# Kernel tuning notes

Hardware: AMD Instinct MI355X
Metric: run time of the kernel (lower is better)

Reference implementation:

```python
import jax, jax.numpy as jnp
import numpy as np

N = 8192        # number of nodes (adjacency is N x N)
F_IN = 256      # in_features
F_OUT = 256     # out_features


def setup_inputs() -> dict:
    key = jax.random.key(0)
    k_x, k_adj, k_kernel, k_bias, k_beta = jax.random.split(key, 5)
    x = jax.random.normal(k_x, (N, F_IN), dtype=jnp.float32)
    adj = jax.random.uniform(k_adj, (N, N), dtype=jnp.float32)  # dense non-negative adjacency buffer
    # xavier-uniform-like scale for the kernel
    limit = float(np.sqrt(6.0 / (F_IN + F_OUT)))
    kernel = jax.random.uniform(k_kernel, (F_IN, F_OUT), dtype=jnp.float32, minval=-limit, maxval=limit)
    bias = 0.01 * jax.random.normal(k_bias, (F_OUT,), dtype=jnp.float32)
    beta = 0.01 * jax.random.normal(k_beta, (N,), dtype=jnp.float32)
    return {"x": x, "adj": adj, "kernel": kernel, "bias": bias, "beta": beta}


def reference(x, adj, kernel, bias, beta):
    # Original: diag(1/(rowsum(adj)+beta)) @ (adj + diag(beta)) @ x @ kernel + bias
    # Fused form: row-scale and diagonal-add applied without materializing NxN diag matrices.
    scale = jnp.reciprocal(jnp.sum(adj, axis=1) + beta)          # [N]
    agg = adj @ x + beta[:, None] * x                             # (adj + diag(beta)) @ x  -> [N, F_IN]
    return (scale[:, None] * agg) @ kernel + bias                 # [N, F_OUT]
```

## Files before the change

kernel.cpp:

```cpp
#include <hip/hip_runtime.h>
#include <hip/hip_bf16.h>


typedef __attribute__((ext_vector_type(8))) short  short8;
typedef __attribute__((ext_vector_type(4))) short  bf16x4;
typedef __attribute__((ext_vector_type(4))) float  floatx4;

#define N_NODES 8192
#define F_DIM   256
#define BK      64
#define NSTEPS  (N_NODES / BK)

#define ASYNC16(g, l)                                                          \
  __builtin_amdgcn_global_load_lds(                                           \
      (const __attribute__((address_space(1))) void*)(g),                     \
      (__attribute__((address_space(3))) void*)(l), 16, 0, 0)

__device__ __forceinline__ unsigned short f2bf(float f) {
  unsigned u = __float_as_uint(f);
  return (unsigned short)((u + 0x7FFFu + ((u >> 16) & 1u)) >> 16);
}

__device__ __forceinline__ short8 pack_bf16x8(floatx4 a, floatx4 b) {
  short8 r;
  r[0] = (short)f2bf(a.x);
  r[1] = (short)f2bf(a.y);
  r[2] = (short)f2bf(a.z);
  r[3] = (short)f2bf(a.w);
  r[4] = (short)f2bf(b.x);
  r[5] = (short)f2bf(b.y);
  r[6] = (short)f2bf(b.z);
  r[7] = (short)f2bf(b.w);
  return r;
}

__global__ __launch_bounds__(256) void tile_bf16_kernel(
    const float* __restrict__ src, unsigned short* __restrict__ dst, int K) {
  const int Nn = F_DIM;
  int cid = blockIdx.x * 256 + threadIdx.x;
  int per_kblk = Nn * 4;
  int kblk = cid / per_kblk;
  int rem  = cid - kblk * per_kblk;
  int n16 = rem >> 6;
  int kg  = (rem >> 4) & 3;
  int nl  = rem & 15;
  int n = n16 * 16 + nl;
  int k = kblk * 32 + kg * 8;
  const float* s = src + (size_t)k * Nn + n;
  floatx4 v0, v1;
  v0.x = s[0];
  v0.y = s[(size_t)Nn];
  v0.z = s[(size_t)2 * Nn];
  v0.w = s[(size_t)3 * Nn];
  v1.x = s[(size_t)4 * Nn];
  v1.y = s[(size_t)5 * Nn];
  v1.z = s[(size_t)6 * Nn];
  v1.w = s[(size_t)7 * Nn];
  *(short8*)(dst + (size_t)cid * 8) = pack_bf16x8(v0, v1);
}

#define MFMA16(a, b, c) __builtin_amdgcn_mfma_f32_16x16x32_bf16(a, b, c, 0, 0, 0)
#define AB(c) (smem + (c) * 4096)

#define LOADB(dst, sv)                                                         \
  _Pragma("unroll") for (int kb_ = 0; kb_ < 2; ++kb_)                          \
  _Pragma("unroll") for (int nf_ = 0; nf_ < 2; ++nf_)                          \
      dst[kb_][nf_] = *(const short8*)(bgl + (size_t)(sv) * 16384 +            \
                                       kb_ * 8192 + nf_ * 512);

#define COPYB()                                                                \
  _Pragma("unroll") for (int kb_ = 0; kb_ < 2; ++kb_)                          \
  _Pragma("unroll") for (int nf_ = 0; nf_ < 2; ++nf_) bc[kb_][nf_] = bn[kb_][nf_];

#define WRITE_A(cw)                                                            \
  {                                                                            \
    rsum += (areg_w.x + areg_w.y) + (areg_w.z + areg_w.w);                     \
    bf16x4 pk_;                                                                \
    pk_[0] = (short)f2bf(areg_w.x);                                            \
    pk_[1] = (short)f2bf(areg_w.y);                                            \
    pk_[2] = (short)f2bf(areg_w.z);                                            \
    pk_[3] = (short)f2bf(areg_w.w);                                            \
    *(bf16x4*)(AB(cw) + awoff) = pk_;                                          \
  }

#define COMPUTE(c)                                                             \
  {                                                                            \
    const char* Ab_ = AB(c);                                                   \
    short8 a00 = *(const short8*)(Ab_ + aoff00);                \
    short8 a01 = *(const short8*)(Ab_ + aoff01);                \
    short8 a10 = *(const short8*)(Ab_ + aoff10);                \
    short8 a11 = *(const short8*)(Ab_ + aoff11);                \
    acc[0][0] = MFMA16(a00, bc[0][0], acc[0][0]);                              \
    acc[0][1] = MFMA16(a00, bc[0][1], acc[0][1]);                              \
    acc[1][0] = MFMA16(a10, bc[0][0], acc[1][0]);                              \
    acc[1][1] = MFMA16(a10, bc[0][1], acc[1][1]);                              \
    acc[0][0] = MFMA16(a01, bc[1][0], acc[0][0]);                              \
    acc[0][1] = MFMA16(a01, bc[1][1], acc[0][1]);                              \
    acc[1][0] = MFMA16(a11, bc[1][0], acc[1][0]);                              \
    acc[1][1] = MFMA16(a11, bc[1][1], acc[1][1]);                              \
  }

#define FULL_ITER(sv, c, cw)                                                   \
  LOADB(bn, (sv) + 1);                                                         \
  areg_l = *(const floatx4*)(agl + (size_t)((sv) + 2) * BK);                   \
  asm volatile("s_waitcnt lgkmcnt(0)\n\ts_barrier" ::: "memory");              \
  WRITE_A(cw);                                                                 \
  COMPUTE(c);                                                                  \
  COPYB();                                                                     \
  areg_w = areg_l;

__global__ __launch_bounds__(512, 2) void fused_kernel(
    const float* __restrict__ adj, const unsigned short* __restrict__ xbt,
    const float* __restrict__ x, const float* __restrict__ beta,
    const float* __restrict__ bias, const unsigned short* __restrict__ wbt,
    float* __restrict__ out) {
  __shared__ __attribute__((aligned(16))) char smem[49408];
  float* sscale = (float*)(smem + 49152);
  float* sbeta  = (float*)(smem + 49280);

  const int tid = threadIdx.x;
  const int w   = tid >> 6;
  const int l   = tid & 63;
  const int kq  = l >> 4;
  const int ml  = l & 15;
  const int m0  = blockIdx.x * 32;

  const int arow = tid >> 4;
  const int ag4  = tid & 15;
  const float* agl = adj + (size_t)(m0 + arow) * N_NODES + ag4 * 4;
  const int awoff = arow * 128 + (((ag4 >> 1) ^ (arow & 7)) << 4) + (ag4 & 1) * 8;

  const int aoff00 = (0 * 16 + ml) * 128 + (((0 * 4 + kq) ^ (ml & 7)) << 4);
  const int aoff01 = (0 * 16 + ml) * 128 + (((1 * 4 + kq) ^ (ml & 7)) << 4);
  const int aoff10 = (1 * 16 + ml) * 128 + (((0 * 4 + kq) ^ (ml & 7)) << 4);
  const int aoff11 = (1 * 16 + ml) * 128 + (((1 * 4 + kq) ^ (ml & 7)) << 4);

  const unsigned short* bgl = xbt + w * 1024 + kq * 128 + ml * 8;

  floatx4 acc[2][2];
  const floatx4 zf4 = {0.f, 0.f, 0.f, 0.f};
  acc[0][0] = zf4; acc[0][1] = zf4; acc[1][0] = zf4; acc[1][1] = zf4;
  float rsum = 0.f;
  floatx4 areg_w, areg_l;
  short8 bc[2][2], bn[2][2];

  {
    floatx4 a0v = *(const floatx4*)(agl);
    LOADB(bc, 0);
    areg_w = *(const floatx4*)(agl + BK);
    rsum += (a0v.x + a0v.y) + (a0v.z + a0v.w);
    bf16x4 pk;
    pk[0] = (short)f2bf(a0v.x);
    pk[1] = (short)f2bf(a0v.y);
    pk[2] = (short)f2bf(a0v.z);
    pk[3] = (short)f2bf(a0v.w);
    *(bf16x4*)(AB(0) + awoff) = pk;
  }

  for (int t = 0; t < 42; ++t) {
    const int s0 = 3 * t;
    FULL_ITER(s0,     0, 1);
    FULL_ITER(s0 + 1, 1, 2);
    FULL_ITER(s0 + 2, 2, 0);
  }
  LOADB(bn, 127);
  asm volatile("s_waitcnt lgkmcnt(0)\n\ts_barrier" ::: "memory");
  WRITE_A(1);
  COMPUTE(0);
  COPYB();
  asm volatile("s_waitcnt lgkmcnt(0)\n\ts_barrier" ::: "memory");
  COMPUTE(1);

  __syncthreads();

  {
    const float* xs = x + (size_t)m0 * F_DIM + tid * 4;
    char* xd = smem + 16384 + (w << 10);
#pragma unroll
    for (int q = 0; q < 4; ++q) ASYNC16(xs + q * 2048, xd + q * 8192);
  }
  {
    float rs = rsum;
    rs += __shfl_xor(rs, 1);
    rs += __shfl_xor(rs, 2);
    rs += __shfl_xor(rs, 4);
    rs += __shfl_xor(rs, 8);
    if ((l & 15) == 0) {
      int row = w * 4 + (l >> 4);
      float b = beta[m0 + row];
      sbeta[row]  = b;
      sscale[row] = 1.0f / (rs + b);
    }
  }
  __syncthreads();

  const float* xl = (const float*)(smem + 16384);
  unsigned short* G = (unsigned short*)smem;
#pragma unroll
  for (int nf = 0; nf < 2; ++nf) {
    int col = w * 32 + nf * 16 + ml;
    int chunk = col >> 3;
#pragma unroll
    for (int mf = 0; mf < 2; ++mf)
#pragma unroll
      for (int r = 0; r < 4; ++r) {
        int row = mf * 16 + kq * 4 + r;
        float g = sscale[row] * (acc[mf][nf][r] + sbeta[row] * xl[row * F_DIM + col]);
        int slot = (chunk & 24) | ((chunk ^ row) & 7);
        G[row * 256 + slot * 8 + (col & 7)] = f2bf(g);
      }
  }
  __syncthreads();

  floatx4 acc2[2][2];
  acc2[0][0] = zf4; acc2[0][1] = zf4; acc2[1][0] = zf4; acc2[1][1] = zf4;
#pragma unroll
  for (int s2 = 0; s2 < 8; ++s2) {
    int c = s2 * 4 + kq;
    int sl = (c & 24) | ((c ^ ml) & 7);
    short8 ag0 = *(const short8*)(G + (ml)      * 256 + sl * 8);
    short8 ag1 = *(const short8*)(G + (16 + ml) * 256 + sl * 8);
    const unsigned short* wb = wbt + s2 * 8192 + (w * 2) * 512 + kq * 128 + ml * 8;
    short8 wv0 = *(const short8*)(wb);
    short8 wv1 = *(const short8*)(wb + 512);
    acc2[0][0] = MFMA16(ag0, wv0, acc2[0][0]);
    acc2[1][0] = MFMA16(ag1, wv0, acc2[1][0]);
    acc2[0][1] = MFMA16(ag0, wv1, acc2[0][1]);
    acc2[1][1] = MFMA16(ag1, wv1, acc2[1][1]);
  }
#pragma unroll
  for (int nf = 0; nf < 2; ++nf) {
    int col = w * 32 + nf * 16 + ml;
    float bv = bias[col];
#pragma unroll
    for (int mf = 0; mf < 2; ++mf)
#pragma unroll
      for (int r = 0; r < 4; ++r) {
        int row = m0 + mf * 16 + kq * 4 + r;
        out[(size_t)row * F_DIM + col] = acc2[mf][nf][r] + bv;
      }
  }
}

extern "C" void kernel_launch(void* const* d_in, const int* in_sizes, int n_in,
                              void* d_out, int out_size, void* d_ws, size_t ws_size,
                              hipStream_t stream) {
  const float* x    = (const float*)d_in[0];
  const float* adj  = (const float*)d_in[1];
  const float* kern = (const float*)d_in[2];
  const float* bias = (const float*)d_in[3];
  const float* beta = (const float*)d_in[4];
  float* out = (float*)d_out;

  char* ws = (char*)d_ws;
  unsigned short* xbt = (unsigned short*)ws;
  unsigned short* wbt = xbt + (size_t)N_NODES * F_DIM;

  tile_bf16_kernel<<<(N_NODES * F_DIM / 8) / 256, 256, 0, stream>>>(x, xbt, N_NODES);
  tile_bf16_kernel<<<(F_DIM * F_DIM / 8) / 256, 256, 0, stream>>>(kern, wbt, F_DIM);
  fused_kernel<<<256, 512, 0, stream>>>(adj, xbt, x, beta, bias, wbt, out);
}
```

Before: 428.5 us.

## Quadruple K-tile depth of adjacency GEMM pipeline and stream B fragments per sub-step

Raises the K tile from 64 to 256, so each barrier-separated stage stages a 32x256 bf16 slice of the adjacency in LDS with a new swizzle, and the main loop drops from 128 steps to 32. Each stage now runs eight MFMA sub-steps, loading B (the pre-transposed bf16 x) from global just-in-time, one sub-step ahead, instead of prefetching a whole stage of B into registers. The aim is fewer barriers and longer MFMA runs per barrier. In exchange the kernel needs about 48KB of LDS for the A buffers, launch bounds drop to one block per CU, and the per-sub-step global B loads may expose latency.

```diff
diff --git a/kernel.cpp b/kernel.cpp
--- a/kernel.cpp
+++ b/kernel.cpp
@@ -3,12 +3,11 @@
 
 
 typedef __attribute__((ext_vector_type(8))) short  short8;
-typedef __attribute__((ext_vector_type(4))) short  bf16x4;
 typedef __attribute__((ext_vector_type(4))) float  floatx4;
 
 #define N_NODES 8192
 #define F_DIM   256
-#define BK      64
+#define BK      256
 #define NSTEPS  (N_NODES / BK)
 
 #define ASYNC16(g, l)                                                          \
@@ -60,56 +59,65 @@
 }
 
 #define MFMA16(a, b, c) __builtin_amdgcn_mfma_f32_16x16x32_bf16(a, b, c, 0, 0, 0)
-#define AB(c) (smem + (c) * 4096)
-
-#define LOADB(dst, sv)                                                         \
-  _Pragma("unroll") for (int kb_ = 0; kb_ < 2; ++kb_)                          \
-  _Pragma("unroll") for (int nf_ = 0; nf_ < 2; ++nf_)                          \
-      dst[kb_][nf_] = *(const short8*)(bgl + (size_t)(sv) * 16384 +            \
-                                       kb_ * 8192 + nf_ * 512);
-
-#define COPYB()                                                                \
-  _Pragma("unroll") for (int kb_ = 0; kb_ < 2; ++kb_)                          \
-  _Pragma("unroll") for (int nf_ = 0; nf_ < 2; ++nf_) bc[kb_][nf_] = bn[kb_][nf_];
+#define AB(c)  (smem + (c) * 16384)
+#define LDB(p) (*(const short8*)(p))
+#define BS(sv) (bgl + (size_t)(sv) * 65536)
+
+#define AOFF(mf, kb)                                                           \
+  (((mf) * 16 + ml) * 512 +                                                    \
+   (((((kb) * 4 + kq) & 24) | ((((kb) * 4 + kq) ^ ml) & 7)) << 4))
 
 #define WRITE_A(cw)                                                            \
   {                                                                            \
-    rsum += (areg_w.x + areg_w.y) + (areg_w.z + areg_w.w);                     \
-    bf16x4 pk_;                                                                \
-    pk_[0] = (short)f2bf(areg_w.x);                                            \
-    pk_[1] = (short)f2bf(areg_w.y);                                            \
-    pk_[2] = (short)f2bf(areg_w.z);                                            \
-    pk_[3] = (short)f2bf(areg_w.w);                                            \
-    *(bf16x4*)(AB(cw) + awoff) = pk_;                                          \
-  }
-
-#define COMPUTE(c)                                                             \
+    rsum += ((aw0.x + aw0.y) + (aw0.z + aw0.w)) +                              \
+            ((aw1.x + aw1.y) + (aw1.z + aw1.w)) +                              \
+            ((aw2.x + aw2.y) + (aw2.z + aw2.w)) +                              \
+            ((aw3.x + aw3.y) + (aw3.z + aw3.w));                               \
+    *(short8*)(AB(cw) + awoff0) = pack_bf16x8(aw0, aw1);                       \
+    *(short8*)(AB(cw) + awoff1) = pack_bf16x8(aw2, aw3);                       \
+  }
+
+#define KB(kb)                                                                 \
+  a0_ = *(const short8*)(Ab_ + AOFF(0, kb));                                   \
+  a1_ = *(const short8*)(Ab_ + AOFF(1, kb));                                   \
+  n0_ = LDB(Bsv_ + ((kb) + 1) * 8192);                                         \
+  n1_ = LDB(Bsv_ + ((kb) + 1) * 8192 + 512);                                   \
+  acc[0][0] = MFMA16(a0_, b0_, acc[0][0]);                                     \
+  acc[0][1] = MFMA16(a0_, b1_, acc[0][1]);                                     \
+  acc[1][0] = MFMA16(a1_, b0_, acc[1][0]);                                     \
+  acc[1][1] = MFMA16(a1_, b1_, acc[1][1]);                                     \
+  b0_ = n0_; b1_ = n1_;
+
+#define KBLAST(kb)                                                             \
+  a0_ = *(const short8*)(Ab_ + AOFF(0, kb));                                   \
+  a1_ = *(const short8*)(Ab_ + AOFF(1, kb));                                   \
+  acc[0][0] = MFMA16(a0_, b0_, acc[0][0]);                                     \
+  acc[0][1] = MFMA16(a0_, b1_, acc[0][1]);                                     \
+  acc[1][0] = MFMA16(a1_, b0_, acc[1][0]);                                     \
+  acc[1][1] = MFMA16(a1_, b1_, acc[1][1]);
+
+#define COMPUTE(c, sv)                                                         \
   {                                                                            \
     const char* Ab_ = AB(c);                                                   \
-    short8 a00 = *(const short8*)(Ab_ + aoff00);                \
-    short8 a01 = *(const short8*)(Ab_ + aoff01);                \
-    short8 a10 = *(const short8*)(Ab_ + aoff10);                \
-    short8 a11 = *(const short8*)(Ab_ + aoff11);                \
-    acc[0][0] = MFMA16(a00, bc[0][0], acc[0][0]);                              \
-    acc[0][1] = MFMA16(a00, bc[0][1], acc[0][1]);                              \
-    acc[1][0] = MFMA16(a10, bc[0][0], acc[1][0]);                              \
-    acc[1][1] = MFMA16(a10, bc[0][1], acc[1][1]);                              \
-    acc[0][0] = MFMA16(a01, bc[1][0], acc[0][0]);                              \
-    acc[0][1] = MFMA16(a01, bc[1][1], acc[0][1]);                              \
-    acc[1][0] = MFMA16(a11, bc[1][0], acc[1][0]);                              \
-    acc[1][1] = MFMA16(a11, bc[1][1], acc[1][1]);                              \
+    const unsigned short* Bsv_ = BS(sv);                                       \
+    short8 b0_ = pb0, b1_ = pb1;                                               \
+    short8 a0_, a1_, n0_, n1_;                                                 \
+    KB(0) KB(1) KB(2) KB(3) KB(4) KB(5) KB(6) KBLAST(7)                        \
   }
 
 #define FULL_ITER(sv, c, cw)                                                   \
-  LOADB(bn, (sv) + 1);                                                         \
-  areg_l = *(const floatx4*)(agl + (size_t)((sv) + 2) * BK);                   \
+  al0 = *(const floatx4*)(agp + (size_t)((sv) + 2) * BK);                      \
+  al1 = *(const floatx4*)(agp + (size_t)((sv) + 2) * BK + 4);                  \
+  al2 = *(const floatx4*)(agp + (size_t)((sv) + 2) * BK + 8);                  \
+  al3 = *(const floatx4*)(agp + (size_t)((sv) + 2) * BK + 12);                 \
+  pb0 = LDB(BS(sv));                                                           \
+  pb1 = LDB(BS(sv) + 512);                                                     \
   asm volatile("s_waitcnt lgkmcnt(0)\n\ts_barrier" ::: "memory");              \
   WRITE_A(cw);                                                                 \
-  COMPUTE(c);                                                                  \
-  COPYB();                                                                     \
-  areg_w = areg_l;
-
-__global__ __launch_bounds__(512, 2) void fused_kernel(
+  COMPUTE(c, sv);                                                              \
+  aw0 = al0; aw1 = al1; aw2 = al2; aw3 = al3;
+
+__global__ __launch_bounds__(512, 1) void fused_kernel(
     const float* __restrict__ adj, const unsigned short* __restrict__ xbt,
     const float* __restrict__ x, const float* __restrict__ beta,
     const float* __restrict__ bias, const unsigned short* __restrict__ wbt,
@@ -126,14 +134,11 @@
   const int m0  = blockIdx.x * 32;
 
   const int arow = tid >> 4;
-  const int ag4  = tid & 15;
-  const float* agl = adj + (size_t)(m0 + arow) * N_NODES + ag4 * 4;
-  const int awoff = arow * 128 + (((ag4 >> 1) ^ (arow & 7)) << 4) + (ag4 & 1) * 8;
-
-  const int aoff00 = (0 * 16 + ml) * 128 + (((0 * 4 + kq) ^ (ml & 7)) << 4);
-  const int aoff01 = (0 * 16 + ml) * 128 + (((1 * 4 + kq) ^ (ml & 7)) << 4);
-  const int aoff10 = (1 * 16 + ml) * 128 + (((0 * 4 + kq) ^ (ml & 7)) << 4);
-  const int aoff11 = (1 * 16 + ml) * 128 + (((1 * 4 + kq) ^ (ml & 7)) << 4);
+  const int aq   = tid & 15;
+  const float* agp = adj + (size_t)(m0 + arow) * N_NODES + aq * 16;
+  const int j0 = aq * 2, j1 = aq * 2 + 1;
+  const int awoff0 = arow * 512 + (((j0 & 24) | ((j0 ^ arow) & 7)) << 4);
+  const int awoff1 = arow * 512 + (((j1 & 24) | ((j1 ^ arow) & 7)) << 4);
 
   const unsigned short* bgl = xbt + w * 1024 + kq * 128 + ml * 8;
 
@@ -141,35 +146,34 @@
   const floatx4 zf4 = {0.f, 0.f, 0.f, 0.f};
   acc[0][0] = zf4; acc[0][1] = zf4; acc[1][0] = zf4; acc[1][1] = zf4;
   float rsum = 0.f;
-  floatx4 areg_w, areg_l;
-  short8 bc[2][2], bn[2][2];
-
-  {
-    floatx4 a0v = *(const floatx4*)(agl);
-    LOADB(bc, 0);
-    areg_w = *(const floatx4*)(agl + BK);
-    rsum += (a0v.x + a0v.y) + (a0v.z + a0v.w);
-    bf16x4 pk;
-    pk[0] = (short)f2bf(a0v.x);
-    pk[1] = (short)f2bf(a0v.y);
-    pk[2] = (short)f2bf(a0v.z);
-    pk[3] = (short)f2bf(a0v.w);
-    *(bf16x4*)(AB(0) + awoff) = pk;
-  }
-
-  for (int t = 0; t < 42; ++t) {
+  floatx4 aw0, aw1, aw2, aw3, al0, al1, al2, al3;
+  short8 pb0, pb1;
+
+  aw0 = *(const floatx4*)(agp);
+  aw1 = *(const floatx4*)(agp + 4);
+  aw2 = *(const floatx4*)(agp + 8);
+  aw3 = *(const floatx4*)(agp + 12);
+  WRITE_A(0);
+  aw0 = *(const floatx4*)(agp + BK);
+  aw1 = *(const floatx4*)(agp + BK + 4);
+  aw2 = *(const floatx4*)(agp + BK + 8);
+  aw3 = *(const floatx4*)(agp + BK + 12);
+
+  for (int t = 0; t < 10; ++t) {
     const int s0 = 3 * t;
     FULL_ITER(s0,     0, 1);
     FULL_ITER(s0 + 1, 1, 2);
     FULL_ITER(s0 + 2, 2, 0);
   }
-  LOADB(bn, 127);
+  pb0 = LDB(BS(30));
+  pb1 = LDB(BS(30) + 512);
   asm volatile("s_waitcnt lgkmcnt(0)\n\ts_barrier" ::: "memory");
   WRITE_A(1);
-  COMPUTE(0);
-  COPYB();
+  COMPUTE(0, 30);
+  pb0 = LDB(BS(31));
+  pb1 = LDB(BS(31) + 512);
   asm volatile("s_waitcnt lgkmcnt(0)\n\ts_barrier" ::: "memory");
-  COMPUTE(1);
+  COMPUTE(1, 31);
 
   __syncthreads();
 
```

New measurement: 417.9 us. -2.5%, faster.
